# Optimization experiments

Measured on AMD Instinct MI355X. Metric: run time of the kernel, lower is better.

The kernel has to match this reference:

```python
import jax, jax.numpy as jnp
import numpy as np

N, E, C, RB, H = 10000, 160000, 64, 8, 64
AVG_NEIGH = 16.0


def _sph(v):
    # component-normalized real spherical harmonics l=1,2,3 of unit vectors v [E,3]
    x, y, z = v[..., 0], v[..., 1], v[..., 2]
    s3, s5, s15 = 3.0 ** 0.5, 5.0 ** 0.5, 15.0 ** 0.5
    y1 = s3 * jnp.stack([x, y, z], -1)  # [E,3]
    y2 = jnp.stack([
        s15 * x * y,
        s15 * y * z,
        0.5 * s5 * (3.0 * z * z - 1.0),
        s15 * x * z,
        0.5 * s15 * (x * x - y * y),
    ], -1)  # [E,5]
    c1 = (35.0 / 8.0) ** 0.5
    c2 = 105.0 ** 0.5
    c3 = (21.0 / 8.0) ** 0.5
    c4 = (7.0 ** 0.5) / 2.0
    y3 = jnp.stack([
        c1 * y * (3.0 * x * x - y * y),
        c2 * x * y * z,
        c3 * y * (5.0 * z * z - 1.0),
        c4 * z * (5.0 * z * z - 3.0),
        c3 * x * (5.0 * z * z - 1.0),
        0.5 * c2 * z * (x * x - y * y),
        c1 * x * (x * x - y * y),
    ], -1)  # [E,7]
    return y1, y2, y3


def setup_inputs() -> dict:
    key = jax.random.key(0)
    ks = jax.random.split(key, 12)
    inp = {
        'vectors': jax.random.normal(ks[0], (E, 3), jnp.float32),
        'node_feats': jax.random.normal(ks[1], (N, C), jnp.float32),
        'radial_embedding': jax.random.normal(ks[2], (E, RB), jnp.float32),
        'W_up': jax.random.normal(ks[3], (C, C), jnp.float32) / np.sqrt(C),
        'mlp_w1': jax.random.normal(ks[4], (RB, H), jnp.float32) / np.sqrt(RB),
        'mlp_w2': jax.random.normal(ks[5], (H, H), jnp.float32) / np.sqrt(H),
        'mlp_w3': jax.random.normal(ks[6], (H, H), jnp.float32) / np.sqrt(H),
        'mlp_w4': jax.random.normal(ks[7], (H, 4 * C), jnp.float32) / np.sqrt(H),
        'W_down': jax.random.normal(ks[8], (4, C, C), jnp.float32) / np.sqrt(C),
        'senders': jax.random.randint(ks[9], (E,), 0, N, jnp.int32),
        'receivers': jax.random.randint(ks[10], (E,), 0, N, jnp.int32),
    }
    return inp


def reference(vectors, node_feats, radial_embedding, W_up, mlp_w1, mlp_w2, mlp_w3, mlp_w4, W_down, senders, receivers):
    n = node_feats.shape[0]
    # linear_up (scalars: plain channel mixing)
    x = node_feats @ W_up                                   # [N,C]
    sf = x[senders]                                         # [E,C] gather
    u = vectors / (jnp.linalg.norm(vectors, axis=-1, keepdims=True) + 1e-12)
    y1, y2, y3 = _sph(u)
    # radial MLP -> per-irrep mixing weights [E, 4C]
    h = jax.nn.silu(radial_embedding @ mlp_w1)
    h = jax.nn.silu(h @ mlp_w2)
    h = jax.nn.silu(h @ mlp_w3)
    mix = h @ mlp_w4
    m0, m1, m2, m3 = jnp.split(mix, 4, axis=-1)             # each [E,C]
    # tensor product of Cx0e with Y_l -> Cx(l), scaled by radial mix
    msg0 = sf * m0                                          # [E,C]
    msg1 = (sf * m1)[:, :, None] * y1[:, None, :]           # [E,C,3]
    msg2 = (sf * m2)[:, :, None] * y2[:, None, :]           # [E,C,5]
    msg3 = (sf * m3)[:, :, None] * y3[:, None, :]           # [E,C,7]
    inv = 1.0 / jnp.sqrt(jnp.asarray(AVG_NEIGH, msg0.dtype))
    seg = lambda m: jax.ops.segment_sum(m, receivers, num_segments=n) * inv
    o0, o1, o2, o3 = seg(msg0), seg(msg1), seg(msg2), seg(msg3)
    # linear_down: per-l channel mixing
    o0 = o0 @ W_down[0]
    o1 = jnp.einsum('ncm,cd->ndm', o1, W_down[1])
    o2 = jnp.einsum('ncm,cd->ndm', o2, W_down[2])
    o3 = jnp.einsum('ncm,cd->ndm', o3, W_down[3])
    return jnp.concatenate([o0, o1.reshape(n, -1), o2.reshape(n, -1), o3.reshape(n, -1)], axis=-1)  # [N, 16C]
```

## Files before the change

### kernel.cpp

```cpp
#include <hip/hip_runtime.h>
#include <math.h>

#define CC 64
typedef _Float16 f16;
typedef _Float16 half8_t __attribute__((ext_vector_type(8)));
typedef float f32x4 __attribute__((ext_vector_type(4)));

__device__ __forceinline__ float silu_f(float v) {
    return v / (1.0f + __expf(-v));
}

__global__ void k_up(const float* __restrict__ nf, const float* __restrict__ Wup,
                     float* __restrict__ x, int N) {
    int tid = blockIdx.x * blockDim.x + threadIdx.x;
    if (tid >= N * CC) return;
    int n = tid >> 6;
    int j = tid & 63;
    const float* nfr = nf + (size_t)n * CC;
    float acc = 0.f;
#pragma unroll
    for (int k = 0; k < CC; ++k) acc += nfr[k] * Wup[k * CC + j];
    x[tid] = acc;
}

__global__ void k_hist(const int* __restrict__ rcv, int* __restrict__ cnt, int E) {
    int e = blockIdx.x * blockDim.x + threadIdx.x;
    if (e < E) atomicAdd(&cnt[rcv[e]], 1);
}

__global__ __launch_bounds__(1024) void k_scan(const int* __restrict__ cnt,
        int* __restrict__ off, int* __restrict__ cur, int N) {
    __shared__ int wsum[16];
    __shared__ int carry;
    int t = threadIdx.x;
    int wave = t >> 6, lane = t & 63;
    if (t == 0) carry = 0;
    __syncthreads();
    for (int base = 0; base < N; base += 1024) {
        int i = base + t;
        int v = (i < N) ? cnt[i] : 0;
        int sc = v;
#pragma unroll
        for (int d = 1; d < 64; d <<= 1) {
            int u = __shfl_up(sc, d, 64);
            if (lane >= d) sc += u;
        }
        if (lane == 63) wsum[wave] = sc;
        __syncthreads();
        if (wave == 0) {
            int w = (lane < 16) ? wsum[lane] : 0;
            int s2 = w;
#pragma unroll
            for (int d = 1; d < 16; d <<= 1) {
                int u = __shfl_up(s2, d, 64);
                if (lane >= d) s2 += u;
            }
            if (lane < 16) wsum[lane] = s2;
        }
        __syncthreads();
        int wexcl = (wave == 0) ? 0 : wsum[wave - 1];
        int excl = carry + wexcl + (sc - v);
        if (i < N) { off[i] = excl; cur[i] = excl; }
        __syncthreads();
        if (t == 0) carry += wsum[15];
        __syncthreads();
    }
    if (t == 0) off[N] = carry;
}

__global__ void k_fill(const int* __restrict__ rcv, const int* __restrict__ snd,
                       int* __restrict__ cur, int* __restrict__ eid,
                       int* __restrict__ pos, int* __restrict__ sndp, int E) {
    int e = blockIdx.x * blockDim.x + threadIdx.x;
    if (e < E) {
        int p = atomicAdd(&cur[rcv[e]], 1);
        eid[p] = e;
        pos[e] = p;
        sndp[p] = snd[e];
    }
}

__global__ void k_sph(const int* __restrict__ eid, const float* __restrict__ vec,
                      float* __restrict__ yb, int E) {
    int i = blockIdx.x * blockDim.x + threadIdx.x;
    if (i >= E) return;
    int e = eid[i];
    float vx = vec[(size_t)e * 3 + 0];
    float vy = vec[(size_t)e * 3 + 1];
    float vz = vec[(size_t)e * 3 + 2];
    float nrm = sqrtf(vx * vx + vy * vy + vz * vz) + 1e-12f;
    float rinv = 1.0f / nrm;
    float ux = vx * rinv, uy = vy * rinv, uz = vz * rinv;

    const float s3 = 1.7320508075688772f;
    const float s5 = 2.2360679774997896f;
    const float s15 = 3.8729833462074170f;
    const float c1 = 2.0916500663351889f;
    const float c2 = 10.246950765959598f;
    const float c3 = 1.6201851746019651f;
    const float c4 = 1.3228756555322954f;

    float zz = uz * uz, xx = ux * ux, yy = uy * uy;
    float4 r0 = {1.0f, s3 * ux, s3 * uy, s3 * uz};
    float4 r1 = {s15 * ux * uy, s15 * uy * uz, 0.5f * s5 * (3.f * zz - 1.f),
                 s15 * ux * uz};
    float4 r2 = {0.5f * s15 * (xx - yy), c1 * uy * (3.f * xx - yy),
                 c2 * ux * uy * uz, c3 * uy * (5.f * zz - 1.f)};
    float4 r3 = {c4 * uz * (5.f * zz - 3.f), c3 * ux * (5.f * zz - 1.f),
                 0.5f * c2 * uz * (xx - yy), c1 * ux * (xx - yy)};
    float* yr = yb + (size_t)i * 16;
    *(float4*)(yr + 0)  = r0;
    *(float4*)(yr + 4)  = r1;
    *(float4*)(yr + 8)  = r2;
    *(float4*)(yr + 12) = r3;
}

__global__ __launch_bounds__(256) void k_mlp(const float* __restrict__ rad,
        const float* __restrict__ w1, const float* __restrict__ w2,
        const float* __restrict__ w3, const float* __restrict__ w4,
        const int* __restrict__ pos, f16* __restrict__ mixp, int E) {
    __shared__ f16 wB[64][72];
    __shared__ f16 wC[64][72];
    __shared__ f16 act[128][72];

    int t = threadIdx.x;
    int e0 = blockIdx.x * 128;
    int lane = t & 63;
    int wid = t >> 6;

    {
        int n = t & 63;
        int k0 = t >> 6;
        for (int k = k0; k < 64; k += 4) {
            wB[n][k] = (f16)w2[k * 64 + n];
            wC[n][k] = (f16)w3[k * 64 + n];
        }
    }

    {
        int i = t & 127;
        int jh = (t >> 7) * 32;
        int e = e0 + i;
        float r[8];
        if (e < E) {
#pragma unroll
            for (int k = 0; k < 8; ++k) r[k] = rad[(size_t)e * 8 + k];
        } else {
#pragma unroll
            for (int k = 0; k < 8; ++k) r[k] = 0.f;
        }
        float a[32];
#pragma unroll
        for (int j = 0; j < 32; ++j) a[j] = 0.f;
#pragma unroll
        for (int k = 0; k < 8; ++k) {
            float rv = r[k];
#pragma unroll
            for (int j = 0; j < 32; ++j) a[j] += rv * w1[k * 64 + jh + j];
        }
#pragma unroll
        for (int jj = 0; jj < 32; jj += 8) {
            half8_t h;
#pragma unroll
            for (int u = 0; u < 8; ++u) h[u] = (f16)silu_f(a[jj + u]);
            *(half8_t*)&act[i][jh + jj] = h;
        }
    }
    __syncthreads();

    int m0 = wid * 32;
    int fm = lane & 15;
    int q  = lane >> 4;

    auto loadA = [&](int mbase, int kc) -> half8_t {
        return *(const half8_t*)&act[mbase + fm][kc + q * 8];
    };

    {
        half8_t a00 = loadA(m0, 0),      a01 = loadA(m0, 32);
        half8_t a10 = loadA(m0 + 16, 0), a11 = loadA(m0 + 16, 32);
#pragma unroll
        for (int nt = 0; nt < 4; ++nt) {
            half8_t b0 = *(const half8_t*)&wB[nt * 16 + fm][q * 8];
            half8_t b1 = *(const half8_t*)&wB[nt * 16 + fm][32 + q * 8];
            f32x4 c0 = {0.f, 0.f, 0.f, 0.f};
            c0 = __builtin_amdgcn_mfma_f32_16x16x32_f16(a00, b0, c0, 0, 0, 0);
            c0 = __builtin_amdgcn_mfma_f32_16x16x32_f16(a01, b1, c0, 0, 0, 0);
            f32x4 c1 = {0.f, 0.f, 0.f, 0.f};
            c1 = __builtin_amdgcn_mfma_f32_16x16x32_f16(a10, b0, c1, 0, 0, 0);
            c1 = __builtin_amdgcn_mfma_f32_16x16x32_f16(a11, b1, c1, 0, 0, 0);
#pragma unroll
            for (int r = 0; r < 4; ++r) {
                act[m0 + q * 4 + r][nt * 16 + fm]      = (f16)silu_f(c0[r]);
                act[m0 + 16 + q * 4 + r][nt * 16 + fm] = (f16)silu_f(c1[r]);
            }
        }
    }

    {
        half8_t a00 = loadA(m0, 0),      a01 = loadA(m0, 32);
        half8_t a10 = loadA(m0 + 16, 0), a11 = loadA(m0 + 16, 32);
#pragma unroll
        for (int nt = 0; nt < 4; ++nt) {
            half8_t b0 = *(const half8_t*)&wC[nt * 16 + fm][q * 8];
            half8_t b1 = *(const half8_t*)&wC[nt * 16 + fm][32 + q * 8];
            f32x4 c0 = {0.f, 0.f, 0.f, 0.f};
            c0 = __builtin_amdgcn_mfma_f32_16x16x32_f16(a00, b0, c0, 0, 0, 0);
            c0 = __builtin_amdgcn_mfma_f32_16x16x32_f16(a01, b1, c0, 0, 0, 0);
            f32x4 c1 = {0.f, 0.f, 0.f, 0.f};
            c1 = __builtin_amdgcn_mfma_f32_16x16x32_f16(a10, b0, c1, 0, 0, 0);
            c1 = __builtin_amdgcn_mfma_f32_16x16x32_f16(a11, b1, c1, 0, 0, 0);
#pragma unroll
            for (int r = 0; r < 4; ++r) {
                act[m0 + q * 4 + r][nt * 16 + fm]      = (f16)silu_f(c0[r]);
                act[m0 + 16 + q * 4 + r][nt * 16 + fm] = (f16)silu_f(c1[r]);
            }
        }
    }

    half8_t A00 = loadA(m0, 0),      A01 = loadA(m0, 32);
    half8_t A10 = loadA(m0 + 16, 0), A11 = loadA(m0 + 16, 32);

    auto do_l = [&](int l, f16 (*w)[72]) {
#pragma unroll
        for (int nt = 0; nt < 4; ++nt) {
            half8_t b0 = *(const half8_t*)&w[nt * 16 + fm][q * 8];
            half8_t b1 = *(const half8_t*)&w[nt * 16 + fm][32 + q * 8];
            f32x4 c0 = {0.f, 0.f, 0.f, 0.f};
            c0 = __builtin_amdgcn_mfma_f32_16x16x32_f16(A00, b0, c0, 0, 0, 0);
            c0 = __builtin_amdgcn_mfma_f32_16x16x32_f16(A01, b1, c0, 0, 0, 0);
            f32x4 c1 = {0.f, 0.f, 0.f, 0.f};
            c1 = __builtin_amdgcn_mfma_f32_16x16x32_f16(A10, b0, c1, 0, 0, 0);
            c1 = __builtin_amdgcn_mfma_f32_16x16x32_f16(A11, b1, c1, 0, 0, 0);
#pragma unroll
            for (int r = 0; r < 4; ++r) {
                act[m0 + q * 4 + r][nt * 16 + fm]      = (f16)c0[r];
                act[m0 + 16 + q * 4 + r][nt * 16 + fm] = (f16)c1[r];
            }
        }
#pragma unroll
        for (int it = 0; it < 4; ++it) {
            int row = (lane >> 3) + it * 8;
            int er = e0 + m0 + row;
            if (er < E) {
                int p = pos[er];
                half8_t v = *(const half8_t*)&act[m0 + row][(lane & 7) * 8];
                *(half8_t*)&mixp[(size_t)p * 256 + l * 64 + (lane & 7) * 8] = v;
            }
        }
    };

    __syncthreads();
    {
        int n = t & 63;
        int k0 = t >> 6;
        for (int k = k0; k < 64; k += 4) {
            wB[n][k] = (f16)w4[k * 256 + n];
            wC[n][k] = (f16)w4[k * 256 + 64 + n];
        }
    }
    __syncthreads();
    do_l(0, wB);
    do_l(1, wC);
    __syncthreads();
    {
        int n = t & 63;
        int k0 = t >> 6;
        for (int k = k0; k < 64; k += 4) {
            wB[n][k] = (f16)w4[k * 256 + 128 + n];
            wC[n][k] = (f16)w4[k * 256 + 192 + n];
        }
    }
    __syncthreads();
    do_l(2, wB);
    do_l(3, wC);
}

__global__ __launch_bounds__(256) void k_gather(const float* __restrict__ x,
        const f16* __restrict__ mixp, const float* __restrict__ yb,
        const int* __restrict__ sndp, const int* __restrict__ off,
        const float* __restrict__ Wd, float* __restrict__ out, int N) {
    __shared__ float sbuf[4][1024];
    int wv = threadIdx.x >> 6;
    int lane = threadIdx.x & 63;
    int n = blockIdx.x * 4 + wv;
    if (n >= N) return;

    float o[16];
#pragma unroll
    for (int i = 0; i < 16; ++i) o[i] = 0.f;

    auto process = [&](int i) {
        int s = sndp[i];
        const float* yr = yb + (size_t)i * 16;
        float4 A = *(const float4*)(yr + 0);
        float4 B = *(const float4*)(yr + 4);
        float4 Cv = *(const float4*)(yr + 8);
        float4 D = *(const float4*)(yr + 12);
        float sf = x[(size_t)s * 64 + lane];
        const f16* mr = mixp + (size_t)i * 256;
        float t0 = sf * (float)mr[lane];
        float t1 = sf * (float)mr[64 + lane];
        float t2 = sf * (float)mr[128 + lane];
        float t3 = sf * (float)mr[192 + lane];
        o[0]  += t0;
        o[1]  += t1 * A.y;
        o[2]  += t1 * A.z;
        o[3]  += t1 * A.w;
        o[4]  += t2 * B.x;
        o[5]  += t2 * B.y;
        o[6]  += t2 * B.z;
        o[7]  += t2 * B.w;
        o[8]  += t2 * Cv.x;
        o[9]  += t3 * Cv.y;
        o[10] += t3 * Cv.z;
        o[11] += t3 * Cv.w;
        o[12] += t3 * D.x;
        o[13] += t3 * D.y;
        o[14] += t3 * D.z;
        o[15] += t3 * D.w;
    };

    int beg = off[n], end = off[n + 1];
    int i = beg;
    for (; i + 1 < end; i += 2) { process(i); process(i + 1); }
    if (i < end) process(i);

#pragma unroll
    for (int t = 0; t < 16; ++t) sbuf[wv][t * 64 + lane] = o[t];

    float d[16];
#pragma unroll
    for (int i2 = 0; i2 < 16; ++i2) d[i2] = 0.f;
#pragma unroll 1
    for (int c = 0; c < 64; ++c) {
        float w0 = Wd[c * 64 + lane];
        float w1r = Wd[4096 + c * 64 + lane];
        float w2r = Wd[8192 + c * 64 + lane];
        float w3r = Wd[12288 + c * 64 + lane];
        const float* sb = &sbuf[wv][c];
        d[0] += sb[0] * w0;
#pragma unroll
        for (int m = 0; m < 3; ++m) d[1 + m] += sb[(1 + m) * 64] * w1r;
#pragma unroll
        for (int m = 0; m < 5; ++m) d[4 + m] += sb[(4 + m) * 64] * w2r;
#pragma unroll
        for (int m = 0; m < 7; ++m) d[9 + m] += sb[(9 + m) * 64] * w3r;
    }

    float* outr = out + (size_t)n * 1024;
    outr[lane] = 0.25f * d[0];
#pragma unroll
    for (int m = 0; m < 3; ++m) outr[64 + lane * 3 + m] = 0.25f * d[1 + m];
#pragma unroll
    for (int m = 0; m < 5; ++m) outr[256 + lane * 5 + m] = 0.25f * d[4 + m];
#pragma unroll
    for (int m = 0; m < 7; ++m) outr[576 + lane * 7 + m] = 0.25f * d[9 + m];
}

extern "C" void kernel_launch(void* const* d_in, const int* in_sizes, int n_in,
                              void* d_out, int out_size, void* d_ws, size_t ws_size,
                              hipStream_t stream) {
    const float* vectors    = (const float*)d_in[0];
    const float* node_feats = (const float*)d_in[1];
    const float* radial     = (const float*)d_in[2];
    const float* W_up       = (const float*)d_in[3];
    const float* w1         = (const float*)d_in[4];
    const float* w2         = (const float*)d_in[5];
    const float* w3         = (const float*)d_in[6];
    const float* w4         = (const float*)d_in[7];
    const float* Wd         = (const float*)d_in[8];
    const int*   snd        = (const int*)d_in[9];
    const int*   rcv        = (const int*)d_in[10];
    float* out = (float*)d_out;

    int E = in_sizes[9];
    int N = in_sizes[1] / CC;

    float* ws   = (float*)d_ws;
    float* x    = ws;
    float* yb   = x + (size_t)N * 64;
    f16*   mixp = (f16*)(yb + (size_t)E * 16);
    int*   cnt  = (int*)((char*)mixp + (size_t)E * 256 * sizeof(f16));
    int*   off  = cnt + N;
    int*   cur  = off + (N + 1);
    int*   eid  = cur + N;
    int*   pos  = eid + E;
    int*   sndp = pos + E;

    hipMemsetAsync(cnt, 0, (size_t)N * sizeof(int), stream);

    k_up<<<(N * CC + 255) / 256, 256, 0, stream>>>(node_feats, W_up, x, N);
    k_hist<<<(E + 255) / 256, 256, 0, stream>>>(rcv, cnt, E);
    k_scan<<<1, 1024, 0, stream>>>(cnt, off, cur, N);
    k_fill<<<(E + 255) / 256, 256, 0, stream>>>(rcv, snd, cur, eid, pos, sndp, E);
    k_sph<<<(E + 255) / 256, 256, 0, stream>>>(eid, vectors, yb, E);
    k_mlp<<<(E + 127) / 128, 256, 0, stream>>>(radial, w1, w2, w3, w4, pos, mixp, E);
    k_gather<<<(N + 3) / 4, 256, 0, stream>>>(x, mixp, yb, sndp, off, Wd, out, N);
}
```

Measured before the change: 253.7 us.

## Fuse spherical harmonics into fill, rework scan and quarter-wave gather

The scan becomes a single pass: each thread sums a contiguous chunk, then the chunk totals are scanned, which replaces the looped block scan. The spherical-harmonics computation moves into the fill kernel and writes directly at the sorted position, removing the separate kernel and the eid array. The gather kernel now gives each 16-lane group of a wave one node, with each lane handling 4 channels through vector loads. The per-node down projection is then done by the whole wave in turn through padded shared memory. This trades more per-lane registers and a serialized down-projection loop for fewer launches and wider memory accesses.

```diff
diff --git a/kernel.cpp b/kernel.cpp
--- a/kernel.cpp
+++ b/kernel.cpp
@@ -4,6 +4,7 @@
 #define CC 64
 typedef _Float16 f16;
 typedef _Float16 half8_t __attribute__((ext_vector_type(8)));
+typedef _Float16 half4_t __attribute__((ext_vector_type(4)));
 typedef float f32x4 __attribute__((ext_vector_type(4)));
 
 __device__ __forceinline__ float silu_f(float v) {
@@ -31,60 +32,53 @@
 __global__ __launch_bounds__(1024) void k_scan(const int* __restrict__ cnt,
         int* __restrict__ off, int* __restrict__ cur, int N) {
     __shared__ int wsum[16];
-    __shared__ int carry;
     int t = threadIdx.x;
     int wave = t >> 6, lane = t & 63;
-    if (t == 0) carry = 0;
-    __syncthreads();
-    for (int base = 0; base < N; base += 1024) {
-        int i = base + t;
-        int v = (i < N) ? cnt[i] : 0;
-        int sc = v;
-#pragma unroll
-        for (int d = 1; d < 64; d <<= 1) {
-            int u = __shfl_up(sc, d, 64);
-            if (lane >= d) sc += u;
-        }
-        if (lane == 63) wsum[wave] = sc;
-        __syncthreads();
-        if (wave == 0) {
-            int w = (lane < 16) ? wsum[lane] : 0;
-            int s2 = w;
-#pragma unroll
-            for (int d = 1; d < 16; d <<= 1) {
-                int u = __shfl_up(s2, d, 64);
-                if (lane >= d) s2 += u;
-            }
-            if (lane < 16) wsum[lane] = s2;
-        }
-        __syncthreads();
-        int wexcl = (wave == 0) ? 0 : wsum[wave - 1];
-        int excl = carry + wexcl + (sc - v);
-        if (i < N) { off[i] = excl; cur[i] = excl; }
-        __syncthreads();
-        if (t == 0) carry += wsum[15];
-        __syncthreads();
-    }
-    if (t == 0) off[N] = carry;
+    int per = (N + 1023) >> 10;
+    int i0 = t * per;
+    int s = 0;
+    for (int j = 0; j < per; ++j) {
+        int i = i0 + j;
+        if (i < N) s += cnt[i];
+    }
+    int sc = s;
+#pragma unroll
+    for (int d = 1; d < 64; d <<= 1) {
+        int u = __shfl_up(sc, d, 64);
+        if (lane >= d) sc += u;
+    }
+    if (lane == 63) wsum[wave] = sc;
+    __syncthreads();
+    if (wave == 0) {
+        int v = (lane < 16) ? wsum[lane] : 0;
+        int s2 = v;
+#pragma unroll
+        for (int d = 1; d < 16; d <<= 1) {
+            int u = __shfl_up(s2, d, 64);
+            if (lane >= d) s2 += u;
+        }
+        if (lane < 16) wsum[lane] = s2;
+    }
+    __syncthreads();
+    int base = ((wave > 0) ? wsum[wave - 1] : 0) + (sc - s);
+    int run = base;
+    for (int j = 0; j < per; ++j) {
+        int i = i0 + j;
+        if (i < N) { off[i] = run; cur[i] = run; run += cnt[i]; }
+    }
+    if (t == 1023) off[N] = run;
 }
 
 __global__ void k_fill(const int* __restrict__ rcv, const int* __restrict__ snd,
-                       int* __restrict__ cur, int* __restrict__ eid,
-                       int* __restrict__ pos, int* __restrict__ sndp, int E) {
+                       const float* __restrict__ vec, int* __restrict__ cur,
+                       int* __restrict__ pos, int* __restrict__ sndp,
+                       float* __restrict__ yb, int E) {
     int e = blockIdx.x * blockDim.x + threadIdx.x;
-    if (e < E) {
-        int p = atomicAdd(&cur[rcv[e]], 1);
-        eid[p] = e;
-        pos[e] = p;
-        sndp[p] = snd[e];
-    }
-}
-
-__global__ void k_sph(const int* __restrict__ eid, const float* __restrict__ vec,
-                      float* __restrict__ yb, int E) {
-    int i = blockIdx.x * blockDim.x + threadIdx.x;
-    if (i >= E) return;
-    int e = eid[i];
+    if (e >= E) return;
+    int p = atomicAdd(&cur[rcv[e]], 1);
+    pos[e] = p;
+    sndp[p] = snd[e];
+
     float vx = vec[(size_t)e * 3 + 0];
     float vy = vec[(size_t)e * 3 + 1];
     float vz = vec[(size_t)e * 3 + 2];
@@ -108,7 +102,7 @@
                  c2 * ux * uy * uz, c3 * uy * (5.f * zz - 1.f)};
     float4 r3 = {c4 * uz * (5.f * zz - 3.f), c3 * ux * (5.f * zz - 1.f),
                  0.5f * c2 * uz * (xx - yy), c1 * ux * (xx - yy)};
-    float* yr = yb + (size_t)i * 16;
+    float* yr = yb + (size_t)p * 16;
     *(float4*)(yr + 0)  = r0;
     *(float4*)(yr + 4)  = r1;
     *(float4*)(yr + 8)  = r2;
@@ -276,33 +270,44 @@
     do_l(3, wC);
 }
 
-__global__ __launch_bounds__(256) void k_gather(const float* __restrict__ x,
+#define GW 2
+__global__ __launch_bounds__(128) void k_gather(const float* __restrict__ x,
         const f16* __restrict__ mixp, const float* __restrict__ yb,
         const int* __restrict__ sndp, const int* __restrict__ off,
         const float* __restrict__ Wd, float* __restrict__ out, int N) {
-    __shared__ float sbuf[4][1024];
+    __shared__ float sbuf[GW][1296];
     int wv = threadIdx.x >> 6;
     int lane = threadIdx.x & 63;
-    int n = blockIdx.x * 4 + wv;
-    if (n >= N) return;
-
-    float o[16];
-#pragma unroll
-    for (int i = 0; i < 16; ++i) o[i] = 0.f;
-
-    auto process = [&](int i) {
+    int g = lane >> 4;
+    int cl = lane & 15;
+    int c0 = cl * 4;
+    int nb = blockIdx.x * (GW * 4) + wv * 4;
+    int n = nb + g;
+    int beg = 0, end = 0;
+    if (n < N) { beg = off[n]; end = off[n + 1]; }
+
+    f32x4 o[16];
+#pragma unroll
+    for (int m = 0; m < 16; ++m) o[m] = (f32x4){0.f, 0.f, 0.f, 0.f};
+
+#pragma unroll 2
+    for (int i = beg; i < end; ++i) {
         int s = sndp[i];
+        const f16* mr = mixp + (size_t)i * 256 + c0;
+        half4_t h0 = *(const half4_t*)(mr);
+        half4_t h1 = *(const half4_t*)(mr + 64);
+        half4_t h2 = *(const half4_t*)(mr + 128);
+        half4_t h3 = *(const half4_t*)(mr + 192);
+        f32x4 sf = *(const f32x4*)&x[(size_t)s * 64 + c0];
         const float* yr = yb + (size_t)i * 16;
-        float4 A = *(const float4*)(yr + 0);
-        float4 B = *(const float4*)(yr + 4);
-        float4 Cv = *(const float4*)(yr + 8);
-        float4 D = *(const float4*)(yr + 12);
-        float sf = x[(size_t)s * 64 + lane];
-        const f16* mr = mixp + (size_t)i * 256;
-        float t0 = sf * (float)mr[lane];
-        float t1 = sf * (float)mr[64 + lane];
-        float t2 = sf * (float)mr[128 + lane];
-        float t3 = sf * (float)mr[192 + lane];
+        f32x4 A  = *(const f32x4*)(yr + 0);
+        f32x4 B  = *(const f32x4*)(yr + 4);
+        f32x4 Cv = *(const f32x4*)(yr + 8);
+        f32x4 D  = *(const f32x4*)(yr + 12);
+        f32x4 t0 = sf * (f32x4){(float)h0.x, (float)h0.y, (float)h0.z, (float)h0.w};
+        f32x4 t1 = sf * (f32x4){(float)h1.x, (float)h1.y, (float)h1.z, (float)h1.w};
+        f32x4 t2 = sf * (f32x4){(float)h2.x, (float)h2.y, (float)h2.z, (float)h2.w};
+        f32x4 t3 = sf * (f32x4){(float)h3.x, (float)h3.y, (float)h3.z, (float)h3.w};
         o[0]  += t0;
         o[1]  += t1 * A.y;
         o[2]  += t1 * A.z;
@@ -319,43 +324,64 @@
         o[13] += t3 * D.y;
         o[14] += t3 * D.z;
         o[15] += t3 * D.w;
-    };
-
-    int beg = off[n], end = off[n + 1];
-    int i = beg;
-    for (; i + 1 < end; i += 2) { process(i); process(i + 1); }
-    if (i < end) process(i);
-
-#pragma unroll
-    for (int t = 0; t < 16; ++t) sbuf[wv][t * 64 + lane] = o[t];
-
-    float d[16];
-#pragma unroll
-    for (int i2 = 0; i2 < 16; ++i2) d[i2] = 0.f;
+    }
+
+    float* sw = sbuf[wv];
 #pragma unroll 1
-    for (int c = 0; c < 64; ++c) {
-        float w0 = Wd[c * 64 + lane];
-        float w1r = Wd[4096 + c * 64 + lane];
-        float w2r = Wd[8192 + c * 64 + lane];
-        float w3r = Wd[12288 + c * 64 + lane];
-        const float* sb = &sbuf[wv][c];
-        d[0] += sb[0] * w0;
-#pragma unroll
-        for (int m = 0; m < 3; ++m) d[1 + m] += sb[(1 + m) * 64] * w1r;
-#pragma unroll
-        for (int m = 0; m < 5; ++m) d[4 + m] += sb[(4 + m) * 64] * w2r;
-#pragma unroll
-        for (int m = 0; m < 7; ++m) d[9 + m] += sb[(9 + m) * 64] * w3r;
-    }
-
-    float* outr = out + (size_t)n * 1024;
-    outr[lane] = 0.25f * d[0];
-#pragma unroll
-    for (int m = 0; m < 3; ++m) outr[64 + lane * 3 + m] = 0.25f * d[1 + m];
-#pragma unroll
-    for (int m = 0; m < 5; ++m) outr[256 + lane * 5 + m] = 0.25f * d[4 + m];
-#pragma unroll
-    for (int m = 0; m < 7; ++m) outr[576 + lane * 7 + m] = 0.25f * d[9 + m];
+    for (int gg = 0; gg < 4; ++gg) {
+        if (g == gg) {
+#pragma unroll
+            for (int j = 0; j < 4; ++j) {
+#pragma unroll
+                for (int a = 0; a < 4; ++a) {
+                    f32x4 vq = {o[4 * a + 0][j], o[4 * a + 1][j],
+                                o[4 * a + 2][j], o[4 * a + 3][j]};
+                    *(f32x4*)&sw[(c0 + j) * 20 + 4 * a] = vq;
+                }
+            }
+        }
+        int ng = nb + gg;
+        if (ng < N) {
+            float dm[16];
+#pragma unroll
+            for (int m2 = 0; m2 < 16; ++m2) dm[m2] = 0.f;
+#pragma unroll 1
+            for (int c = 0; c < 64; ++c) {
+                f32x4 q0 = *(const f32x4*)&sw[c * 20 + 0];
+                f32x4 q1 = *(const f32x4*)&sw[c * 20 + 4];
+                f32x4 q2 = *(const f32x4*)&sw[c * 20 + 8];
+                f32x4 q3 = *(const f32x4*)&sw[c * 20 + 12];
+                float w0  = Wd[c * 64 + lane];
+                float w1r = Wd[4096 + c * 64 + lane];
+                float w2r = Wd[8192 + c * 64 + lane];
+                float w3r = Wd[12288 + c * 64 + lane];
+                dm[0]  += q0[0] * w0;
+                dm[1]  += q0[1] * w1r;
+                dm[2]  += q0[2] * w1r;
+                dm[3]  += q0[3] * w1r;
+                dm[4]  += q1[0] * w2r;
+                dm[5]  += q1[1] * w2r;
+                dm[6]  += q1[2] * w2r;
+                dm[7]  += q1[3] * w2r;
+                dm[8]  += q2[0] * w2r;
+                dm[9]  += q2[1] * w3r;
+                dm[10] += q2[2] * w3r;
+                dm[11] += q2[3] * w3r;
+                dm[12] += q3[0] * w3r;
+                dm[13] += q3[1] * w3r;
+                dm[14] += q3[2] * w3r;
+                dm[15] += q3[3] * w3r;
+            }
+            float* outr = out + (size_t)ng * 1024;
+            outr[lane] = 0.25f * dm[0];
+#pragma unroll
+            for (int m2 = 0; m2 < 3; ++m2) outr[64 + lane * 3 + m2] = 0.25f * dm[1 + m2];
+#pragma unroll
+            for (int m2 = 0; m2 < 5; ++m2) outr[256 + lane * 5 + m2] = 0.25f * dm[4 + m2];
+#pragma unroll
+            for (int m2 = 0; m2 < 7; ++m2) outr[576 + lane * 7 + m2] = 0.25f * dm[9 + m2];
+        }
+    }
 }
 
 extern "C" void kernel_launch(void* const* d_in, const int* in_sizes, int n_in,
@@ -384,8 +410,7 @@
     int*   cnt  = (int*)((char*)mixp + (size_t)E * 256 * sizeof(f16));
     int*   off  = cnt + N;
     int*   cur  = off + (N + 1);
-    int*   eid  = cur + N;
-    int*   pos  = eid + E;
+    int*   pos  = cur + N;
     int*   sndp = pos + E;
 
     hipMemsetAsync(cnt, 0, (size_t)N * sizeof(int), stream);
@@ -393,8 +418,7 @@
     k_up<<<(N * CC + 255) / 256, 256, 0, stream>>>(node_feats, W_up, x, N);
     k_hist<<<(E + 255) / 256, 256, 0, stream>>>(rcv, cnt, E);
     k_scan<<<1, 1024, 0, stream>>>(cnt, off, cur, N);
-    k_fill<<<(E + 255) / 256, 256, 0, stream>>>(rcv, snd, cur, eid, pos, sndp, E);
-    k_sph<<<(E + 255) / 256, 256, 0, stream>>>(eid, vectors, yb, E);
+    k_fill<<<(E + 255) / 256, 256, 0, stream>>>(rcv, snd, vectors, cur, pos, sndp, yb, E);
     k_mlp<<<(E + 127) / 128, 256, 0, stream>>>(radial, w1, w2, w3, w4, pos, mixp, E);
-    k_gather<<<(N + 3) / 4, 256, 0, stream>>>(x, mixp, yb, sndp, off, Wd, out, N);
-}
+    k_gather<<<(N + GW * 4 - 1) / (GW * 4), GW * 64, 0, stream>>>(x, mixp, yb, sndp, off, Wd, out, N);
+}
```

Measured after the change: 305.5 us. +20.4%, slower.

## Fuse spherical harmonics into fill, gather-read MLP inputs, and vectorize down-projection

Applied to the files above, without the earlier changes.

The scan becomes a single pass where each thread serially sums a contiguous chunk, replacing the multi-iteration loop with its barriers. The spherical-harmonics kernel is folded into the CSR fill kernel, which writes harmonics directly at the sorted position, and the pos array is dropped. The MLP now reads radial inputs through eid and writes mix rows contiguously instead of scattering through pos. The gather epilogue stores per-lane coefficients in a padded transposed shared layout so the down-projection uses float4 LDS reads and vector FMAs.

```diff
diff --git a/kernel.cpp b/kernel.cpp
--- a/kernel.cpp
+++ b/kernel.cpp
@@ -31,60 +31,53 @@
 __global__ __launch_bounds__(1024) void k_scan(const int* __restrict__ cnt,
         int* __restrict__ off, int* __restrict__ cur, int N) {
     __shared__ int wsum[16];
-    __shared__ int carry;
     int t = threadIdx.x;
     int wave = t >> 6, lane = t & 63;
-    if (t == 0) carry = 0;
-    __syncthreads();
-    for (int base = 0; base < N; base += 1024) {
-        int i = base + t;
-        int v = (i < N) ? cnt[i] : 0;
-        int sc = v;
-#pragma unroll
-        for (int d = 1; d < 64; d <<= 1) {
-            int u = __shfl_up(sc, d, 64);
-            if (lane >= d) sc += u;
-        }
-        if (lane == 63) wsum[wave] = sc;
-        __syncthreads();
-        if (wave == 0) {
-            int w = (lane < 16) ? wsum[lane] : 0;
-            int s2 = w;
-#pragma unroll
-            for (int d = 1; d < 16; d <<= 1) {
-                int u = __shfl_up(s2, d, 64);
-                if (lane >= d) s2 += u;
-            }
-            if (lane < 16) wsum[lane] = s2;
-        }
-        __syncthreads();
-        int wexcl = (wave == 0) ? 0 : wsum[wave - 1];
-        int excl = carry + wexcl + (sc - v);
-        if (i < N) { off[i] = excl; cur[i] = excl; }
-        __syncthreads();
-        if (t == 0) carry += wsum[15];
-        __syncthreads();
-    }
-    if (t == 0) off[N] = carry;
+    int per = (N + 1023) >> 10;
+    int i0 = t * per;
+    int s = 0;
+    for (int j = 0; j < per; ++j) {
+        int i = i0 + j;
+        if (i < N) s += cnt[i];
+    }
+    int sc = s;
+#pragma unroll
+    for (int d = 1; d < 64; d <<= 1) {
+        int u = __shfl_up(sc, d, 64);
+        if (lane >= d) sc += u;
+    }
+    if (lane == 63) wsum[wave] = sc;
+    __syncthreads();
+    if (wave == 0) {
+        int v = (lane < 16) ? wsum[lane] : 0;
+        int s2 = v;
+#pragma unroll
+        for (int d = 1; d < 16; d <<= 1) {
+            int u = __shfl_up(s2, d, 64);
+            if (lane >= d) s2 += u;
+        }
+        if (lane < 16) wsum[lane] = s2;
+    }
+    __syncthreads();
+    int base = ((wave > 0) ? wsum[wave - 1] : 0) + (sc - s);
+    int run = base;
+    for (int j = 0; j < per; ++j) {
+        int i = i0 + j;
+        if (i < N) { off[i] = run; cur[i] = run; run += cnt[i]; }
+    }
+    if (t == 1023) off[N] = run;
 }
 
 __global__ void k_fill(const int* __restrict__ rcv, const int* __restrict__ snd,
-                       int* __restrict__ cur, int* __restrict__ eid,
-                       int* __restrict__ pos, int* __restrict__ sndp, int E) {
+                       const float* __restrict__ vec, int* __restrict__ cur,
+                       int* __restrict__ eid, int* __restrict__ sndp,
+                       float* __restrict__ yb, int E) {
     int e = blockIdx.x * blockDim.x + threadIdx.x;
-    if (e < E) {
-        int p = atomicAdd(&cur[rcv[e]], 1);
-        eid[p] = e;
-        pos[e] = p;
-        sndp[p] = snd[e];
-    }
-}
-
-__global__ void k_sph(const int* __restrict__ eid, const float* __restrict__ vec,
-                      float* __restrict__ yb, int E) {
-    int i = blockIdx.x * blockDim.x + threadIdx.x;
-    if (i >= E) return;
-    int e = eid[i];
+    if (e >= E) return;
+    int p = atomicAdd(&cur[rcv[e]], 1);
+    eid[p] = e;
+    sndp[p] = snd[e];
+
     float vx = vec[(size_t)e * 3 + 0];
     float vy = vec[(size_t)e * 3 + 1];
     float vz = vec[(size_t)e * 3 + 2];
@@ -108,7 +101,7 @@
                  c2 * ux * uy * uz, c3 * uy * (5.f * zz - 1.f)};
     float4 r3 = {c4 * uz * (5.f * zz - 3.f), c3 * ux * (5.f * zz - 1.f),
                  0.5f * c2 * uz * (xx - yy), c1 * ux * (xx - yy)};
-    float* yr = yb + (size_t)i * 16;
+    float* yr = yb + (size_t)p * 16;
     *(float4*)(yr + 0)  = r0;
     *(float4*)(yr + 4)  = r1;
     *(float4*)(yr + 8)  = r2;
@@ -118,7 +111,7 @@
 __global__ __launch_bounds__(256) void k_mlp(const float* __restrict__ rad,
         const float* __restrict__ w1, const float* __restrict__ w2,
         const float* __restrict__ w3, const float* __restrict__ w4,
-        const int* __restrict__ pos, f16* __restrict__ mixp, int E) {
+        const int* __restrict__ eid, f16* __restrict__ mixp, int E) {
     __shared__ f16 wB[64][72];
     __shared__ f16 wC[64][72];
     __shared__ f16 act[128][72];
@@ -140,9 +133,10 @@
     {
         int i = t & 127;
         int jh = (t >> 7) * 32;
-        int e = e0 + i;
+        int ci = e0 + i;
         float r[8];
-        if (e < E) {
+        if (ci < E) {
+            int e = eid[ci];
 #pragma unroll
             for (int k = 0; k < 8; ++k) r[k] = rad[(size_t)e * 8 + k];
         } else {
@@ -241,11 +235,10 @@
 #pragma unroll
         for (int it = 0; it < 4; ++it) {
             int row = (lane >> 3) + it * 8;
-            int er = e0 + m0 + row;
-            if (er < E) {
-                int p = pos[er];
+            int ci = e0 + m0 + row;
+            if (ci < E) {
                 half8_t v = *(const half8_t*)&act[m0 + row][(lane & 7) * 8];
-                *(half8_t*)&mixp[(size_t)p * 256 + l * 64 + (lane & 7) * 8] = v;
+                *(half8_t*)&mixp[(size_t)ci * 256 + l * 64 + (lane & 7) * 8] = v;
             }
         }
     };
@@ -280,7 +273,7 @@
         const f16* __restrict__ mixp, const float* __restrict__ yb,
         const int* __restrict__ sndp, const int* __restrict__ off,
         const float* __restrict__ Wd, float* __restrict__ out, int N) {
-    __shared__ float sbuf[4][1024];
+    __shared__ float sbuf[4][64 * 20];
     int wv = threadIdx.x >> 6;
     int lane = threadIdx.x & 63;
     int n = blockIdx.x * 4 + wv;
@@ -326,36 +319,48 @@
     for (; i + 1 < end; i += 2) { process(i); process(i + 1); }
     if (i < end) process(i);
 
-#pragma unroll
-    for (int t = 0; t < 16; ++t) sbuf[wv][t * 64 + lane] = o[t];
-
-    float d[16];
-#pragma unroll
-    for (int i2 = 0; i2 < 16; ++i2) d[i2] = 0.f;
+    float* sw = sbuf[wv];
+#pragma unroll
+    for (int a = 0; a < 4; ++a) {
+        f32x4 vq = {o[4 * a + 0], o[4 * a + 1], o[4 * a + 2], o[4 * a + 3]};
+        *(f32x4*)&sw[lane * 20 + 4 * a] = vq;
+    }
+
+    f32x4 dA = {0.f, 0.f, 0.f, 0.f}, dB = dA, dC = dA, dD = dA;
 #pragma unroll 1
     for (int c = 0; c < 64; ++c) {
-        float w0 = Wd[c * 64 + lane];
+        f32x4 q0 = *(const f32x4*)&sw[c * 20 + 0];
+        f32x4 q1 = *(const f32x4*)&sw[c * 20 + 4];
+        f32x4 q2 = *(const f32x4*)&sw[c * 20 + 8];
+        f32x4 q3 = *(const f32x4*)&sw[c * 20 + 12];
+        float w0  = Wd[c * 64 + lane];
         float w1r = Wd[4096 + c * 64 + lane];
         float w2r = Wd[8192 + c * 64 + lane];
         float w3r = Wd[12288 + c * 64 + lane];
-        const float* sb = &sbuf[wv][c];
-        d[0] += sb[0] * w0;
-#pragma unroll
-        for (int m = 0; m < 3; ++m) d[1 + m] += sb[(1 + m) * 64] * w1r;
-#pragma unroll
-        for (int m = 0; m < 5; ++m) d[4 + m] += sb[(4 + m) * 64] * w2r;
-#pragma unroll
-        for (int m = 0; m < 7; ++m) d[9 + m] += sb[(9 + m) * 64] * w3r;
+        f32x4 wA = {w0, w1r, w1r, w1r};
+        f32x4 wC4 = {w2r, w3r, w3r, w3r};
+        dA += q0 * wA;
+        dB += q1 * w2r;
+        dC += q2 * wC4;
+        dD += q3 * w3r;
     }
 
     float* outr = out + (size_t)n * 1024;
-    outr[lane] = 0.25f * d[0];
-#pragma unroll
-    for (int m = 0; m < 3; ++m) outr[64 + lane * 3 + m] = 0.25f * d[1 + m];
-#pragma unroll
-    for (int m = 0; m < 5; ++m) outr[256 + lane * 5 + m] = 0.25f * d[4 + m];
-#pragma unroll
-    for (int m = 0; m < 7; ++m) outr[576 + lane * 7 + m] = 0.25f * d[9 + m];
+    outr[lane] = 0.25f * dA[0];
+#pragma unroll
+    for (int m = 0; m < 3; ++m) outr[64 + lane * 3 + m] = 0.25f * dA[1 + m];
+    outr[256 + lane * 5 + 0] = 0.25f * dB[0];
+    outr[256 + lane * 5 + 1] = 0.25f * dB[1];
+    outr[256 + lane * 5 + 2] = 0.25f * dB[2];
+    outr[256 + lane * 5 + 3] = 0.25f * dB[3];
+    outr[256 + lane * 5 + 4] = 0.25f * dC[0];
+    outr[576 + lane * 7 + 0] = 0.25f * dC[1];
+    outr[576 + lane * 7 + 1] = 0.25f * dC[2];
+    outr[576 + lane * 7 + 2] = 0.25f * dC[3];
+    outr[576 + lane * 7 + 3] = 0.25f * dD[0];
+    outr[576 + lane * 7 + 4] = 0.25f * dD[1];
+    outr[576 + lane * 7 + 5] = 0.25f * dD[2];
+    outr[576 + lane * 7 + 6] = 0.25f * dD[3];
 }
 
 extern "C" void kernel_launch(void* const* d_in, const int* in_sizes, int n_in,
@@ -385,16 +390,14 @@
     int*   off  = cnt + N;
     int*   cur  = off + (N + 1);
     int*   eid  = cur + N;
-    int*   pos  = eid + E;
-    int*   sndp = pos + E;
+    int*   sndp = eid + E;
 
     hipMemsetAsync(cnt, 0, (size_t)N * sizeof(int), stream);
 
     k_up<<<(N * CC + 255) / 256, 256, 0, stream>>>(node_feats, W_up, x, N);
     k_hist<<<(E + 255) / 256, 256, 0, stream>>>(rcv, cnt, E);
     k_scan<<<1, 1024, 0, stream>>>(cnt, off, cur, N);
-    k_fill<<<(E + 255) / 256, 256, 0, stream>>>(rcv, snd, cur, eid, pos, sndp, E);
-    k_sph<<<(E + 255) / 256, 256, 0, stream>>>(eid, vectors, yb, E);
-    k_mlp<<<(E + 127) / 128, 256, 0, stream>>>(radial, w1, w2, w3, w4, pos, mixp, E);
+    k_fill<<<(E + 255) / 256, 256, 0, stream>>>(rcv, snd, vectors, cur, eid, sndp, yb, E);
+    k_mlp<<<(E + 127) / 128, 256, 0, stream>>>(radial, w1, w2, w3, w4, eid, mixp, E);
     k_gather<<<(N + 3) / 4, 256, 0, stream>>>(x, mixp, yb, sndp, off, Wd, out, N);
 }
```

New measurement: 248.1 us. 2.2% less time.
